# Kernel optimization log

Hardware: AMD Instinct MI355X
Metric: run time of the kernel (lower is better)

The kernel has to match this reference:

```python
import jax, jax.numpy as jnp
import numpy as np
import math

# Static config derived from init_kwargs
B, L, D, H, NL = 256, 256, 128, 2, 2
E = D // H                       # 64
F = L // 2 + 1                   # 129 rfft bins
SR = 0.6                         # sample_ratio (> 1/n_layers)
STEP = (F * (1.0 - SR)) // (NL - 1)          # 51.0, python float floor-div as in torch code
LEFTS = [int(F * (1.0 - SR) - k * STEP) for k in range(NL)]   # [51, 0]
RIGHTS = [int(F - k * STEP) for k in range(NL)]               # [129, 78]
TOPK = max(int(1 * math.log(L)), 1)          # factor=1 -> 5
NUM_TOTAL = 100000                           # user_num + item_num
SPATIAL_RATIO = 0.1
INV_SQRT_E = 1.0 / math.sqrt(E)
INV_SQRT_2 = 1.0 / math.sqrt(2.0)


def setup_inputs() -> dict:
    key = jax.random.key(0)
    ks = jax.random.split(key, 12)
    s = 0.05
    return {
        "paths": jax.random.randint(ks[0], (B, L), 0, NUM_TOTAL),
        "lengths": jax.random.randint(ks[1], (B,), 1, L + 1),
        "degrees": jax.random.randint(ks[2], (B,), 0, 64),
        "training": 1,
        "ego_emb": jax.random.normal(ks[3], (NUM_TOTAL + 1, D), jnp.float32) * s,
        "pos_emb": jax.random.normal(ks[4], (L, D), jnp.float32) * s,
        "Wq": jax.random.normal(ks[5], (NL, D, D), jnp.float32) * s,
        "Wk": jax.random.normal(ks[6], (NL, D, D), jnp.float32) * s,
        "Wv": jax.random.normal(ks[7], (NL, D, D), jnp.float32) * s,
        "Wp": jax.random.normal(ks[8], (NL, D, D), jnp.float32) * s,
        "F1": jax.random.normal(ks[9], (NL, D, 2 * D), jnp.float32) * s,
        "F2": jax.random.normal(ks[10], (NL, 2 * D, D), jnp.float32) * s,
    }


def _hybrid_attention(k, x, mask, Wq, Wk, Wv, Wp):
    # project and split heads: [B,H,E,L]
    def proj(W):
        return (x @ W).reshape(B, L, H, E).transpose(0, 2, 3, 1)
    q, kk, v = proj(Wq), proj(Wk), proj(Wv)
    qf = jnp.fft.rfft(q, axis=-1)   # [B,H,E,F] complex
    kf = jnp.fft.rfft(kk, axis=-1)
    vf = jnp.fft.rfft(v, axis=-1)
    l, r = LEFTS[k], RIGHTS[k]
    # frequency-band attention: band-limited cross-correlation (scatter back == zero-pad)
    res = qf[..., l:r] * jnp.conj(kf[..., l:r])
    box = jnp.zeros(qf.shape, dtype=res.dtype).at[..., l:r].set(res)
    corr = jnp.fft.irfft(box, n=L, axis=-1)          # [B,H,E,L]
    mean_value = jnp.mean(corr, axis=(1, 2))         # [B,L]
    # training branch: global topk delays (shared across batch), roll-based aggregation
    _, delays = jax.lax.top_k(jnp.mean(mean_value, axis=0), TOPK)   # [TOPK]
    weights = mean_value[:, delays]                  # [B,TOPK]
    tmp_corr = jax.nn.softmax(weights, axis=-1)      # [B,TOPK]
    # roll(v, -d) along time == gather at (t + d) % L
    idx = (jnp.arange(L)[None, :] + delays[:, None]) % L            # [TOPK,L]
    gathered = v[:, :, :, idx]                       # [B,H,E,TOPK,L]
    freq = jnp.einsum('bhetl,bt->bhel', gathered, tmp_corr)
    freq = freq.transpose(0, 3, 1, 2).reshape(B, L, D)
    # dual-domain: time attention on band-limited signals (std=True -> same band)
    def band_ifft(f):
        padded = jnp.zeros(f.shape, dtype=f.dtype).at[..., l:r].set(f[..., l:r])
        return jnp.fft.irfft(padded, n=L, axis=-1).transpose(0, 1, 3, 2)   # [B,H,L,E]
    qt, kt, vt = band_ifft(qf), band_ifft(kf), band_ifft(vf)
    scores = jnp.einsum('bhqe,bhke->bhqk', qt, kt) * INV_SQRT_E + mask
    att = jax.nn.softmax(scores, axis=-1)
    spatial = jnp.einsum('bhqk,bhke->bhqe', att, vt).transpose(0, 2, 1, 3).reshape(B, L, D)
    out = (1.0 - SPATIAL_RATIO) * freq + SPATIAL_RATIO * spatial
    return out @ Wp + x


def reference(paths, lengths, degrees, training, ego_emb, pos_emb, Wq, Wk, Wv, Wp, F1, F2):
    del degrees, training  # degrees unused; training branch baked in (training=True)
    x = ego_emb[paths] + pos_emb[None, :, :]         # [B,L,D]
    m = (paths < NUM_TOTAL).astype(jnp.float32)
    mask = ((1.0 - m) * -10000.0)[:, None, None, :]  # [B,1,1,L]
    for k in range(NL):
        a = _hybrid_attention(k, x, mask, Wq[k], Wk[k], Wv[k], Wp[k])
        h = a @ F1[k]
        h = h * 0.5 * (1.0 + jax.lax.erf(h * INV_SQRT_2))   # exact GELU
        x = h @ F2[k]
    # gather last valid position per sequence
    return x[jnp.arange(B), lengths - 1]             # [B,D]
```

## Files before the change

### kernel.cpp

```cpp
#include <hip/hip_runtime.h>
#include <math.h>

#define Bn 256
#define Ln 256
#define Dn 128
#define Hn 2
#define En 64
#define NLn 2
#define TOPKn 5
#define NUM_TOTALn 100000
#define BLD (Bn*Ln*Dn)
#define WT_LAYER 147456

using frag_ab = __attribute__((ext_vector_type(8))) short;
using frag_cd = __attribute__((ext_vector_type(4))) float;

__device__ inline short f2bf(float f) {
    union { float f; unsigned u; } c; c.f = f;
    unsigned r = (c.u + 0x7FFFu + ((c.u >> 16) & 1u)) >> 16;
    return (short)r;
}
__device__ inline float bf2f(short s) {
    union { unsigned u; float f; } c; c.u = ((unsigned)(unsigned short)s) << 16;
    return c.f;
}

__global__ void beacon_kernel(float* out, float v) { out[0] = v; }

__global__ __launch_bounds__(256) void build_G_kernel(short* __restrict__ G) {
    int k = blockIdx.x, t = blockIdx.y, s = threadIdx.x;
    int d = (t - s) & 255;
    int f1 = (k == 0) ? 51 : 1;
    int f2 = (k == 0) ? 127 : 77;
    float acc;
    if (d == 0) {
        acc = 2.0f * (float)(f2 - f1 + 1);
    } else {
        const float c = 3.14159265358979323846f / 256.0f;
        int ahi = (d * (2 * f2 + 1)) & 511;
        int alo = (d * (2 * f1 - 1)) & 511;
        acc = (sinf(c * (float)ahi) - sinf(c * (float)alo)) / sinf(c * (float)d);
    }
    acc += (k == 0) ? ((d & 1) ? -1.0f : 1.0f)
                    : 1.0f;
    G[((size_t)k * 256 + t) * 256 + s] = f2bf(acc * (1.0f / 256.0f));
}

__global__ __launch_bounds__(256) void build_x_kernel(const int* __restrict__ paths,
                                                      const float* __restrict__ ego,
                                                      const float* __restrict__ pos,
                                                      short* __restrict__ x) {
    int base = (blockIdx.x * 256 + threadIdx.x) * 4;
    int d = base & 127;
    int bl = base >> 7;
    int t = bl & 255;
    float4 e = *(const float4*)(ego + (size_t)paths[bl] * Dn + d);
    float4 p = *(const float4*)(pos + t * Dn + d);
    short4 s;
    s.x = f2bf(e.x + p.x); s.y = f2bf(e.y + p.y);
    s.z = f2bf(e.z + p.z); s.w = f2bf(e.w + p.w);
    *(short4*)&x[base] = s;
}

__global__ __launch_bounds__(256) void wtrans_all_kernel(
        const float* __restrict__ Wq, const float* __restrict__ Wk,
        const float* __restrict__ Wv, const float* __restrict__ Wp,
        const float* __restrict__ F1, const float* __restrict__ F2,
        short* __restrict__ Wt) {
    int z = blockIdx.y;
    int idx = blockIdx.x * 256 + threadIdx.x;
    short* WtL = Wt + (size_t)z * WT_LAYER;
    if (idx < 65536) {
        int which = idx >> 14, local = idx & 16383;
        const float* src = (which == 0) ? Wq : (which == 1) ? Wk
                         : (which == 2) ? Wv : Wp;
        float scale = (which == 3) ? 0.1f : 1.0f;
        int n = local & 127, k = local >> 7;
        WtL[(which << 14) + n * 128 + k] = f2bf(scale * src[(size_t)z * 16384 + local]);
    } else if (idx < 98304) {
        int local = idx - 65536;
        int n = local & 255, k = local >> 8;
        WtL[65536 + n * 128 + k] = f2bf(F1[(size_t)z * 32768 + local]);
    } else {
        int local = idx - 98304;
        int n = local & 127, k = local >> 7;
        WtL[98304 + n * 256 + k] = f2bf(F2[(size_t)z * 32768 + local]);
    }
}

template<bool BT_FAST, bool GELU_EPI>
__global__ __launch_bounds__(256)
void mfma_gemm_kernel(const short* A, const short* Bp, short* C, const short* R,
                      int K, int lda, int ldb, int ldc, int ldr,
                      long long sA, long long sB, long long sC, long long sR,
                      long long sCsplit, float alpha, float beta) {
    int bz = blockIdx.z;
    A += (size_t)bz * sA; C += (size_t)bz * sC;
    if (R) R += (size_t)bz * sR;
    const short* Bt = Bp + (size_t)bz * sB;
    const int m0 = blockIdx.x * 128, n0 = blockIdx.y * 128;
    int n0c = n0;
    if (sCsplit) { C += (size_t)blockIdx.y * sCsplit; n0c = 0; }
    __shared__ short As[128 * 40];
    __shared__ short Bs[128 * 40];
    int tid = threadIdx.x;
    int lane = tid & 63, wave = tid >> 6;
    int wr = (wave >> 1) * 64, wc = (wave & 1) * 64;
    int l15 = lane & 15, qd = lane >> 4;

    frag_cd zero4 = {0.f, 0.f, 0.f, 0.f};
    frag_cd acc[4][4];
    #pragma unroll
    for (int i = 0; i < 4; i++)
        #pragma unroll
        for (int j = 0; j < 4; j++) acc[i][j] = zero4;

    int arow = tid >> 1, acg = (tid & 1) * 16;
    int bnrow = tid >> 1, bcg = (tid & 1) * 16;
    int bkk = tid & 31, bnb = (tid >> 5) * 16;

    int4 pa0, pa1, pb0, pb1;
    {
        const short* ap = A + (size_t)(m0 + arow) * lda + acg;
        pa0 = *(const int4*)ap; pa1 = *(const int4*)(ap + 8);
        if (BT_FAST) {
            const short* bp = Bt + (size_t)(n0 + bnrow) * ldb + bcg;
            pb0 = *(const int4*)bp; pb1 = *(const int4*)(bp + 8);
        } else {
            const short* bp = Bt + (size_t)bkk * ldb + n0 + bnb;
            pb0 = *(const int4*)bp; pb1 = *(const int4*)(bp + 8);
        }
    }

    for (int k0 = 0; k0 < K; k0 += 32) {
        __syncthreads();
        *(int4*)&As[arow * 40 + acg] = pa0;
        *(int4*)&As[arow * 40 + acg + 8] = pa1;
        if (BT_FAST) {
            *(int4*)&Bs[bnrow * 40 + bcg] = pb0;
            *(int4*)&Bs[bnrow * 40 + bcg + 8] = pb1;
        } else {
            short tmp[16];
            *(int4*)&tmp[0] = pb0; *(int4*)&tmp[8] = pb1;
            #pragma unroll
            for (int i = 0; i < 16; i++) Bs[(bnb + i) * 40 + bkk] = tmp[i];
        }
        __syncthreads();
        if (k0 + 32 < K) {
            const short* ap = A + (size_t)(m0 + arow) * lda + k0 + 32 + acg;
            pa0 = *(const int4*)ap; pa1 = *(const int4*)(ap + 8);
            if (BT_FAST) {
                const short* bp = Bt + (size_t)(n0 + bnrow) * ldb + k0 + 32 + bcg;
                pb0 = *(const int4*)bp; pb1 = *(const int4*)(bp + 8);
            } else {
                const short* bp = Bt + (size_t)(k0 + 32 + bkk) * ldb + n0 + bnb;
                pb0 = *(const int4*)bp; pb1 = *(const int4*)(bp + 8);
            }
        }
        frag_ab af[4], bf[4];
        #pragma unroll
        for (int ms = 0; ms < 4; ms++)
            af[ms] = *(frag_ab*)&As[(wr + ms * 16 + l15) * 40 + qd * 8];
        #pragma unroll
        for (int ns = 0; ns < 4; ns++)
            bf[ns] = *(frag_ab*)&Bs[(wc + ns * 16 + l15) * 40 + qd * 8];
        #pragma unroll
        for (int ms = 0; ms < 4; ms++)
            #pragma unroll
            for (int ns = 0; ns < 4; ns++)
                acc[ms][ns] = __builtin_amdgcn_mfma_f32_16x16x32_bf16(
                    bf[ns], af[ms], acc[ms][ns], 0, 0, 0);
    }
    #pragma unroll
    for (int ms = 0; ms < 4; ms++) {
        int m = m0 + wr + ms * 16 + l15;
        #pragma unroll
        for (int ns = 0; ns < 4; ns++) {
            int nb = wc + ns * 16 + qd * 4;
            float v[4];
            #pragma unroll
            for (int r = 0; r < 4; r++) v[r] = alpha * acc[ms][ns][r];
            if (R) {
                short4 r4 = *(const short4*)&R[(size_t)m * ldr + n0 + nb];
                v[0] += beta * bf2f(r4.x); v[1] += beta * bf2f(r4.y);
                v[2] += beta * bf2f(r4.z); v[3] += beta * bf2f(r4.w);
            }
            if (GELU_EPI) {
                #pragma unroll
                for (int r = 0; r < 4; r++)
                    v[r] = v[r] * 0.5f * (1.0f + erff(v[r] * 0.70710678118654752f));
            }
            short4 o;
            o.x = f2bf(v[0]); o.y = f2bf(v[1]); o.z = f2bf(v[2]); o.w = f2bf(v[3]);
            *(short4*)&C[(size_t)m * ldc + n0c + nb] = o;
        }
    }
}

static inline void mgemm(hipStream_t s, const short* A, const short* B, short* C,
                         const short* R, int M, int N, int K,
                         int lda, int ldb, int ldc, int ldr,
                         long long sA, long long sB, long long sC, long long sR,
                         int batch, float alpha, float beta, bool btFast, bool gelu,
                         long long sCsplit = 0) {
    dim3 grid(M / 128, N / 128, batch), block(256);
    if (btFast) {
        if (gelu) mfma_gemm_kernel<true, true ><<<grid, block, 0, s>>>(A, B, C, R, K, lda, ldb, ldc, ldr, sA, sB, sC, sR, sCsplit, alpha, beta);
        else      mfma_gemm_kernel<true, false><<<grid, block, 0, s>>>(A, B, C, R, K, lda, ldb, ldc, ldr, sA, sB, sC, sR, sCsplit, alpha, beta);
    } else {
        if (gelu) mfma_gemm_kernel<false, true ><<<grid, block, 0, s>>>(A, B, C, R, K, lda, ldb, ldc, ldr, sA, sB, sC, sR, sCsplit, alpha, beta);
        else      mfma_gemm_kernel<false, false><<<grid, block, 0, s>>>(A, B, C, R, K, lda, ldb, ldc, ldr, sA, sB, sC, sR, sCsplit, alpha, beta);
    }
}

template<bool DUAL, bool GELU_EPI, bool MIXA>
__global__ __launch_bounds__(512)
void bgemm_kernel(const short* __restrict__ A1, const short* __restrict__ B1, int K1,
                  const short* __restrict__ A2, const short* __restrict__ B2, int K2,
                  short* C, const short* __restrict__ R, int ldc, int ldr,
                  long long sCsplit,
                  const float* __restrict__ tc, const int* __restrict__ delays) {
    const int m0 = blockIdx.x * 256;
    int n0c;
    if (sCsplit) { C += (size_t)blockIdx.y * sCsplit; n0c = 0; }
    else         { n0c = blockIdx.y * 128; }
    __shared__ short As[256 * 40];
    __shared__ short Bs[128 * 40];
    int tid = threadIdx.x;
    int lane = tid & 63, wave = tid >> 6;
    int wr = (wave & 3) * 64, wc = (wave >> 2) * 64;
    int l15 = lane & 15, qd = lane >> 4;

    float wj[TOPKn]; int dj[TOPKn];
    if (MIXA) {
        #pragma unroll
        for (int j = 0; j < TOPKn; j++) {
            wj[j] = tc[blockIdx.x * TOPKn + j];
            dj[j] = delays[j];
        }
    }

    frag_cd zero4 = {0.f, 0.f, 0.f, 0.f};
    frag_cd acc[4][4];
    #pragma unroll
    for (int i = 0; i < 4; i++)
        #pragma unroll
        for (int j = 0; j < 4; j++) acc[i][j] = zero4;

    int arow = tid >> 1, acg = (tid & 1) * 16;
    int brow = tid >> 2, bcg = (tid & 3) * 8;

    #pragma unroll
    for (int pass = 0; pass < (DUAL ? 2 : 1); pass++) {
        const short* A = pass ? A2 : A1;
        const short* Bb = (pass ? B2 : B1);
        int K = pass ? K2 : K1;
        const bool domix = MIXA && (pass == 0);
        const short* Bt = Bb + (size_t)blockIdx.y * 128 * K;
        const short* xb = A + ((size_t)m0 << 7);
        int4 pa0, pa1, pb0;
        {
            if (!domix) {
                const short* ap = A + (size_t)(m0 + arow) * K + acg;
                pa0 = *(const int4*)ap; pa1 = *(const int4*)(ap + 8);
            }
            pb0 = *(const int4*)(Bt + (size_t)brow * K + bcg);
        }
        for (int k0 = 0; k0 < K; k0 += 32) {
            __syncthreads();
            if (domix) {
                #pragma unroll
                for (int c = 0; c < 2; c++) {
                    int col = k0 + acg + c * 8;
                    float m8[8] = {0.f, 0.f, 0.f, 0.f, 0.f, 0.f, 0.f, 0.f};
                    #pragma unroll
                    for (int j = 0; j < TOPKn; j++) {
                        frag_ab v = *(const frag_ab*)(xb + (((arow + dj[j]) & 255) << 7) + col);
                        #pragma unroll
                        for (int i = 0; i < 8; i++) m8[i] += wj[j] * bf2f(v[i]);
                    }
                    frag_ab o;
                    #pragma unroll
                    for (int i = 0; i < 8; i++) o[i] = f2bf(m8[i]);
                    *(frag_ab*)&As[arow * 40 + acg + c * 8] = o;
                }
            } else {
                *(int4*)&As[arow * 40 + acg] = pa0;
                *(int4*)&As[arow * 40 + acg + 8] = pa1;
            }
            *(int4*)&Bs[brow * 40 + bcg] = pb0;
            __syncthreads();
            if (k0 + 32 < K) {
                if (!domix) {
                    const short* ap = A + (size_t)(m0 + arow) * K + k0 + 32 + acg;
                    pa0 = *(const int4*)ap; pa1 = *(const int4*)(ap + 8);
                }
                pb0 = *(const int4*)(Bt + (size_t)brow * K + k0 + 32 + bcg);
            }
            frag_ab af[4], bf[4];
            #pragma unroll
            for (int ms = 0; ms < 4; ms++)
                af[ms] = *(frag_ab*)&As[(wr + ms * 16 + l15) * 40 + qd * 8];
            #pragma unroll
            for (int ns = 0; ns < 4; ns++)
                bf[ns] = *(frag_ab*)&Bs[(wc + ns * 16 + l15) * 40 + qd * 8];
            #pragma unroll
            for (int ms = 0; ms < 4; ms++)
                #pragma unroll
                for (int ns = 0; ns < 4; ns++)
                    acc[ms][ns] = __builtin_amdgcn_mfma_f32_16x16x32_bf16(
                        bf[ns], af[ms], acc[ms][ns], 0, 0, 0);
        }
    }
    #pragma unroll
    for (int ms = 0; ms < 4; ms++) {
        int m = m0 + wr + ms * 16 + l15;
        #pragma unroll
        for (int ns = 0; ns < 4; ns++) {
            int nb = wc + ns * 16 + qd * 4;
            float v[4];
            #pragma unroll
            for (int r = 0; r < 4; r++) v[r] = acc[ms][ns][r];
            if (R) {
                short4 r4 = *(const short4*)&R[(size_t)m * ldr + n0c + nb];
                v[0] += bf2f(r4.x); v[1] += bf2f(r4.y);
                v[2] += bf2f(r4.z); v[3] += bf2f(r4.w);
            }
            if (GELU_EPI) {
                #pragma unroll
                for (int r = 0; r < 4; r++)
                    v[r] = v[r] * 0.5f * (1.0f + erff(v[r] * 0.70710678118654752f));
            }
            short4 o;
            o.x = f2bf(v[0]); o.y = f2bf(v[1]); o.z = f2bf(v[2]); o.w = f2bf(v[3]);
            *(short4*)&C[(size_t)m * ldc + n0c + nb] = o;
        }
    }
}

__global__ __launch_bounds__(512, 4) void attn_kernel(short* q,
        const short* __restrict__ kb, const short* __restrict__ vf,
        const int* __restrict__ paths, float* __restrict__ mv2) {
    int h = blockIdx.x, b = blockIdx.y;
    __shared__ short SB[256 * 72];
    __shared__ short ks[64 * 72];
    __shared__ short vT[80 * 72];
    __shared__ float masks[256];
    __shared__ float mvpart[512];
    int tid = threadIdx.x;
    int lane = tid & 63, wave = tid >> 6;
    int l15 = lane & 15, qd = lane >> 4;
    if (tid < 256) masks[tid] = (paths[b * 256 + tid] < NUM_TOTALn) ? 0.0f : -10000.0f;
    {
        int e0 = tid * 2;
        #pragma unroll
        for (int i = 0; i < 2; i++) {
            int e = e0 + i;
            int row = 64 + (e >> 6), col = e & 63;
            vT[row * 72 + col] = (row == 64) ? (short)0x3F80 : (short)0;
        }
    }
    short* qg = q + ((size_t)b << 15) + (size_t)h * 64;
    const short* kg = kb + ((size_t)b << 15) + (size_t)h * 64;
    const short* vg = vf + ((size_t)b << 15) + (size_t)h * 64;

    #pragma unroll
    for (int p = 0; p < 4; p++) {
        int chunk = p * 512 + tid;
        int r = chunk >> 3, cb = (chunk & 7) * 8;
        *(frag_ab*)&SB[r * 72 + cb] = *(const frag_ab*)(qg + (size_t)r * 128 + cb);
    }
    __syncthreads();
    int myrow = wave * 32;
    frag_ab aq[2][2];
    #pragma unroll
    for (int mt = 0; mt < 2; mt++)
        #pragma unroll
        for (int hf = 0; hf < 2; hf++)
            aq[mt][hf] = *(frag_ab*)&SB[(myrow + mt * 16 + l15) * 72 + hf * 32 + qd * 8];

    frag_cd zero4 = {0.f, 0.f, 0.f, 0.f};
    frag_cd oacc[2][5];
    #pragma unroll
    for (int mt = 0; mt < 2; mt++)
        #pragma unroll
        for (int et = 0; et < 5; et++) oacc[mt][et] = zero4;
    float macc = 0.0f;
    int tau = tid & 255, half = tid >> 8;

    for (int jt = 0; jt < 4; jt++) {
        __syncthreads();
        {
            int r = tid >> 3, cb = (tid & 7) * 8;
            *(frag_ab*)&ks[r * 72 + cb] =
                *(const frag_ab*)(kg + (size_t)(jt * 64 + r) * 128 + cb);
            frag_ab v8 = *(const frag_ab*)(vg + (size_t)(jt * 64 + r) * 128 + cb);
            int swz = (((r >> 3) ^ (cb >> 3)) << 3) + (r & 7);
            #pragma unroll
            for (int i = 0; i < 8; i++) vT[(cb + i) * 72 + swz] = v8[i];
        }
        __syncthreads();
        #pragma unroll
        for (int mt = 0; mt < 2; mt++) {
            #pragma unroll
            for (int nt = 0; nt < 4; nt++) {
                frag_ab b0 = *(frag_ab*)&ks[(nt * 16 + l15) * 72 + qd * 8];
                frag_ab b1 = *(frag_ab*)&ks[(nt * 16 + l15) * 72 + 32 + qd * 8];
                frag_cd c = zero4;
                c = __builtin_amdgcn_mfma_f32_16x16x32_bf16(aq[mt][0], b0, c, 0, 0, 0);
                c = __builtin_amdgcn_mfma_f32_16x16x32_bf16(aq[mt][1], b1, c, 0, 0, 0);
                int keyLocal = nt * 16 + l15;
                #pragma unroll
                for (int r = 0; r < 4; r++) {
                    int row = myrow + mt * 16 + qd * 4 + r;
                    int tt = (row - jt * 64 - keyLocal) & 255;
                    SB[tt * 66 + keyLocal] = f2bf(c[r] * 0.125f);
                }
            }
        }
        __syncthreads();
        {
            const int* SD32 = (const int*)&SB[tau * 66 + half * 32];
            #pragma unroll
            for (int i = 0; i < 16; i++) {
                int pk = SD32[i];
                macc += bf2f((short)(pk & 0xFFFF)) + bf2f((short)(pk >> 16));
            }
        }
        #pragma unroll
        for (int mt = 0; mt < 2; mt++) {
            int row = myrow + mt * 16 + l15;
            #pragma unroll
            for (int hf = 0; hf < 2; hf++) {
                int kl0 = hf * 32 + qd * 8;
                frag_ab pfrag;
                #pragma unroll
                for (int j = 0; j < 8; j++) {
                    int kl = kl0 + j;
                    int tt = (row - jt * 64 - kl) & 255;
                    float s = bf2f(SB[tt * 66 + kl]);
                    pfrag[j] = f2bf(__expf(s + masks[jt * 64 + kl]));
                }
                #pragma unroll
                for (int et = 0; et < 5; et++) {
                    int e = et * 16 + l15;
                    int blk = (hf * 4 + qd) ^ ((e >> 3) & 7);
                    frag_ab bv = *(frag_ab*)&vT[e * 72 + (blk << 3)];
                    oacc[mt][et] = __builtin_amdgcn_mfma_f32_16x16x32_bf16(pfrag, bv, oacc[mt][et], 0, 0, 0);
                }
            }
        }
    }
    __syncthreads();
    mvpart[tid] = macc;
    __syncthreads();
    if (tid < 256)
        mv2[(size_t)h * 65536 + b * 256 + tid] =
            (mvpart[tid] + mvpart[tid + 256]) * 0.0625f;
    #pragma unroll
    for (int mt = 0; mt < 2; mt++) {
        #pragma unroll
        for (int r = 0; r < 4; r++) {
            float l = oacc[mt][4][r];
            l = __shfl(l, (lane & 48));
            float inv = 1.0f / l;
            int row = myrow + mt * 16 + qd * 4 + r;
            #pragma unroll
            for (int et = 0; et < 4; et++)
                qg[(size_t)row * 128 + et * 16 + l15] = f2bf(oacc[mt][et][r] * inv);
        }
    }
}

__global__ __launch_bounds__(256) void gm_reduce_kernel(const float* __restrict__ mv2,
                                                        float* __restrict__ gm) {
    int tau = blockIdx.x;
    int b = threadIdx.x;
    __shared__ float red[256];
    red[b] = mv2[b * 256 + tau] + mv2[65536 + b * 256 + tau];
    __syncthreads();
    for (int s = 128; s > 0; s >>= 1) { if (b < s) red[b] += red[b + s]; __syncthreads(); }
    if (b == 0) gm[tau] = red[0] * (1.0f / 256.0f);
}

__global__ __launch_bounds__(256) void topk_softmax_kernel(const float* __restrict__ gm,
                                                           const float* __restrict__ mv2,
                                                           int* __restrict__ delays,
                                                           float* __restrict__ tc) {
    __shared__ float vsh[4];
    __shared__ int ish[4];
    __shared__ int dsh[TOPKn];
    int tid = threadIdx.x;
    int lane = tid & 63, wave = tid >> 6;
    float v = gm[tid];
    for (int t = 0; t < TOPKn; t++) {
        float mv_ = v; int mi = tid;
        #pragma unroll
        for (int s = 32; s > 0; s >>= 1) {
            float v2 = __shfl_xor(mv_, s); int i2 = __shfl_xor(mi, s);
            if (v2 > mv_ || (v2 == mv_ && i2 < mi)) { mv_ = v2; mi = i2; }
        }
        if (lane == 0) { vsh[wave] = mv_; ish[wave] = mi; }
        __syncthreads();
        if (tid == 0) {
            float bv = vsh[0]; int bi = ish[0];
            #pragma unroll
            for (int w = 1; w < 4; w++)
                if (vsh[w] > bv || (vsh[w] == bv && ish[w] < bi)) { bv = vsh[w]; bi = ish[w]; }
            dsh[t] = bi; delays[t] = bi;
        }
        __syncthreads();
        if (tid == dsh[t]) v = -1e30f;
    }
    __syncthreads();
    int b = tid;
    float w[TOPKn];
    float m = -1e30f;
    #pragma unroll
    for (int j = 0; j < TOPKn; j++) {
        w[j] = mv2[b * 256 + dsh[j]] + mv2[65536 + b * 256 + dsh[j]];
        m = fmaxf(m, w[j]);
    }
    float ssum = 0.0f;
    #pragma unroll
    for (int j = 0; j < TOPKn; j++) { w[j] = expf(w[j] - m); ssum += w[j]; }
    #pragma unroll
    for (int j = 0; j < TOPKn; j++) tc[b * TOPKn + j] = w[j] / ssum;
}

__global__ __launch_bounds__(256) void gather_out_kernel(const short* __restrict__ x,
                                                         const int* __restrict__ lengths,
                                                         float* __restrict__ out) {
    int idx = blockIdx.x * 256 + threadIdx.x;
    int d = idx & 127;
    int b = idx >> 7;
    out[idx] = bf2f(x[((size_t)b << 15) + (size_t)(lengths[b] - 1) * Dn + d]);
}

extern "C" void kernel_launch(void* const* d_in, const int* in_sizes, int n_in,
                              void* d_out, int out_size, void* d_ws, size_t ws_size,
                              hipStream_t stream) {
    const int* paths    = (const int*)d_in[0];
    const int* lengths  = (const int*)d_in[1];
    const float* ego    = (const float*)d_in[4];
    const float* pos    = (const float*)d_in[5];
    const float* Wq     = (const float*)d_in[6];
    const float* Wk     = (const float*)d_in[7];
    const float* Wv     = (const float*)d_in[8];
    const float* Wp     = (const float*)d_in[9];
    const float* F1     = (const float*)d_in[10];
    const float* F2     = (const float*)d_in[11];
    float* out = (float*)d_out;

    const size_t need = (size_t)5 * BLD * 2 + 131072 * 2 + 131072 * 4
                        + 256 * 4 + 1280 * 4 + 16 * 4 + (size_t)NLn * WT_LAYER * 2;
    if (ws_size < need) {
        beacon_kernel<<<dim3(1), dim3(1), 0, stream>>>(out, (float)(ws_size >> 20));
        return;
    }

    short* x    = (short*)d_ws;
    short* q    = x + (size_t)1 * BLD;
    short* kb   = x + (size_t)2 * BLD;
    short* vf   = x + (size_t)3 * BLD;
    short* x5   = x + (size_t)4 * BLD;
    short* Gb   = x + (size_t)5 * BLD;
    float* mv   = (float*)(Gb + 131072);
    float* gm   = mv + 131072;
    float* tc   = gm + 256;
    int* delays = (int*)(tc + 1280);
    short* Wt   = (short*)(delays + 16);

    build_G_kernel<<<dim3(2, 256), dim3(256), 0, stream>>>(Gb);
    build_x_kernel<<<dim3(BLD / 1024), dim3(256), 0, stream>>>(paths, ego, pos, x);

    wtrans_all_kernel<<<dim3(512, NLn), dim3(256), 0, stream>>>(Wq, Wk, Wv, Wp, F1, F2, Wt);
    mgemm(stream, Wt + 49152, Wt + 32768, Wt + 131072, nullptr,
          128, 128, 128, 128, 128, 128, 0,
          WT_LAYER, WT_LAYER, WT_LAYER, 0, NLn,
          9.0f, 0.0f, false, false);

    for (int k = 0; k < NLn; k++) {
        const short* WtL = Wt + (size_t)k * WT_LAYER;
        mgemm(stream, Gb + (size_t)k * 65536, x, x5, nullptr,
              256, 128, 256, 256, 128, 128, 0,
              0, 32768, 32768, 0, 256, 1.0f, 0.0f, false, false);
        bgemm_kernel<false, false, false><<<dim3(256, 3), dim3(512), 0, stream>>>(
            x5, WtL + 0, 128, nullptr, nullptr, 0, q, nullptr, 128, 0,
            (long long)BLD, nullptr, nullptr);

        attn_kernel<<<dim3(2, 256), dim3(512), 0, stream>>>(q, kb, vf, paths, mv);

        gm_reduce_kernel<<<dim3(256), dim3(256), 0, stream>>>(mv, gm);
        topk_softmax_kernel<<<dim3(1), dim3(256), 0, stream>>>(gm, mv, delays, tc);

        bgemm_kernel<true, false, true><<<dim3(256, 1), dim3(512), 0, stream>>>(
            x, WtL + 131072, 128, q, WtL + 49152, 128, kb, x, 128, 128, 0,
            tc, delays);
        bgemm_kernel<false, true, false><<<dim3(256, 2), dim3(512), 0, stream>>>(
            kb, WtL + 65536, 128, nullptr, nullptr, 0, vf, nullptr, 256, 0, 0,
            nullptr, nullptr);
        bgemm_kernel<false, false, false><<<dim3(256, 1), dim3(512), 0, stream>>>(
            vf, WtL + 98304, 256, nullptr, nullptr, 0, x, nullptr, 128, 0, 0,
            nullptr, nullptr);
    }

    gather_out_kernel<<<dim3((Bn * Dn) / 256), dim3(256), 0, stream>>>(x, lengths, out);
}
```

Measured before the change: 392.5 us.

## Fuse band-filter GEMM with Q/K/V projection, keeping filtered activations in LDS

Replaces the per-batch filter GEMM (G @ x, written to a global x5 buffer) and the following Q/K/V projection GEMM with one kernel per batch element. The filtered 256x128 tile is kept in shared memory and reused for all three projections. This removes a global write and read of the intermediate plus one launch. In exchange it uses much more LDS per block (about 98 KB), which lowers occupancy, and the grid shrinks to 256 blocks that each run the three projections in sequence.

After: 378.4 us. 3.6% less time.

```diff
diff --git a/kernel.cpp b/kernel.cpp
--- a/kernel.cpp
+++ b/kernel.cpp
@@ -213,6 +213,129 @@
     }
 }
 
+__global__ __launch_bounds__(512)
+void filtproj_kernel(const short* __restrict__ G, const short* __restrict__ x,
+                     const short* __restrict__ W, short* __restrict__ q) {
+    int b = blockIdx.x;
+    __shared__ short As[256 * 40];
+    __shared__ short Bs[128 * 40];
+    __shared__ short xf[256 * 136];
+    int tid = threadIdx.x;
+    int lane = tid & 63, wave = tid >> 6;
+    int wr = (wave & 3) * 64, wc = (wave >> 2) * 64;
+    int l15 = lane & 15, qd = lane >> 4;
+    const short* xb = x + ((size_t)b << 15);
+
+    frag_cd zero4 = {0.f, 0.f, 0.f, 0.f};
+    frag_cd acc[4][4];
+    #pragma unroll
+    for (int i = 0; i < 4; i++)
+        #pragma unroll
+        for (int j = 0; j < 4; j++) acc[i][j] = zero4;
+
+    int arow = tid >> 1, acg = (tid & 1) * 16;
+    int bkk = tid & 31, bnb = (tid >> 5) * 16;
+
+    int4 pa0, pa1, pb0, pb1;
+    {
+        const short* ap = G + (size_t)arow * 256 + acg;
+        pa0 = *(const int4*)ap; pa1 = *(const int4*)(ap + 8);
+        if (tid < 256) {
+            const short* bp = xb + (size_t)bkk * 128 + bnb;
+            pb0 = *(const int4*)bp; pb1 = *(const int4*)(bp + 8);
+        }
+    }
+    for (int k0 = 0; k0 < 256; k0 += 32) {
+        __syncthreads();
+        *(int4*)&As[arow * 40 + acg] = pa0;
+        *(int4*)&As[arow * 40 + acg + 8] = pa1;
+        if (tid < 256) {
+            short tmp[16];
+            *(int4*)&tmp[0] = pb0; *(int4*)&tmp[8] = pb1;
+            #pragma unroll
+            for (int i = 0; i < 16; i++) Bs[(bnb + i) * 40 + bkk] = tmp[i];
+        }
+        __syncthreads();
+        if (k0 + 32 < 256) {
+            const short* ap = G + (size_t)arow * 256 + k0 + 32 + acg;
+            pa0 = *(const int4*)ap; pa1 = *(const int4*)(ap + 8);
+            if (tid < 256) {
+                const short* bp = xb + (size_t)(k0 + 32 + bkk) * 128 + bnb;
+                pb0 = *(const int4*)bp; pb1 = *(const int4*)(bp + 8);
+            }
+        }
+        frag_ab af[4], bf[4];
+        #pragma unroll
+        for (int ms = 0; ms < 4; ms++)
+            af[ms] = *(frag_ab*)&As[(wr + ms * 16 + l15) * 40 + qd * 8];
+        #pragma unroll
+        for (int ns = 0; ns < 4; ns++)
+            bf[ns] = *(frag_ab*)&Bs[(wc + ns * 16 + l15) * 40 + qd * 8];
+        #pragma unroll
+        for (int ms = 0; ms < 4; ms++)
+            #pragma unroll
+            for (int ns = 0; ns < 4; ns++)
+                acc[ms][ns] = __builtin_amdgcn_mfma_f32_16x16x32_bf16(
+                    bf[ns], af[ms], acc[ms][ns], 0, 0, 0);
+    }
+    #pragma unroll
+    for (int ms = 0; ms < 4; ms++) {
+        int m = wr + ms * 16 + l15;
+        #pragma unroll
+        for (int ns = 0; ns < 4; ns++) {
+            int nb = wc + ns * 16 + qd * 4;
+            short4 o;
+            o.x = f2bf(acc[ms][ns][0]); o.y = f2bf(acc[ms][ns][1]);
+            o.z = f2bf(acc[ms][ns][2]); o.w = f2bf(acc[ms][ns][3]);
+            *(short4*)&xf[m * 136 + nb] = o;
+        }
+    }
+
+    int brow = tid >> 2, bcg = (tid & 3) * 8;
+    #pragma unroll 1
+    for (int y = 0; y < 3; y++) {
+        const short* Bt = W + y * 16384;
+        #pragma unroll
+        for (int i = 0; i < 4; i++)
+            #pragma unroll
+            for (int j = 0; j < 4; j++) acc[i][j] = zero4;
+        int4 pb = *(const int4*)(Bt + (size_t)brow * 128 + bcg);
+        for (int k0 = 0; k0 < 128; k0 += 32) {
+            __syncthreads();
+            *(int4*)&Bs[brow * 40 + bcg] = pb;
+            __syncthreads();
+            if (k0 + 32 < 128)
+                pb = *(const int4*)(Bt + (size_t)brow * 128 + k0 + 32 + bcg);
+            frag_ab af[4], bf[4];
+            #pragma unroll
+            for (int ms = 0; ms < 4; ms++)
+                af[ms] = *(frag_ab*)&xf[(wr + ms * 16 + l15) * 136 + k0 + qd * 8];
+            #pragma unroll
+            for (int ns = 0; ns < 4; ns++)
+                bf[ns] = *(frag_ab*)&Bs[(wc + ns * 16 + l15) * 40 + qd * 8];
+            #pragma unroll
+            for (int ms = 0; ms < 4; ms++)
+                #pragma unroll
+                for (int ns = 0; ns < 4; ns++)
+                    acc[ms][ns] = __builtin_amdgcn_mfma_f32_16x16x32_bf16(
+                        bf[ns], af[ms], acc[ms][ns], 0, 0, 0);
+        }
+        short* Cy = q + (size_t)y * BLD + ((size_t)b << 15);
+        #pragma unroll
+        for (int ms = 0; ms < 4; ms++) {
+            int m = wr + ms * 16 + l15;
+            #pragma unroll
+            for (int ns = 0; ns < 4; ns++) {
+                int nb = wc + ns * 16 + qd * 4;
+                short4 o;
+                o.x = f2bf(acc[ms][ns][0]); o.y = f2bf(acc[ms][ns][1]);
+                o.z = f2bf(acc[ms][ns][2]); o.w = f2bf(acc[ms][ns][3]);
+                *(short4*)&Cy[(size_t)m * 128 + nb] = o;
+            }
+        }
+    }
+}
+
 template<bool DUAL, bool GELU_EPI, bool MIXA>
 __global__ __launch_bounds__(512)
 void bgemm_kernel(const short* __restrict__ A1, const short* __restrict__ B1, int K1,
@@ -582,12 +705,8 @@
 
     for (int k = 0; k < NLn; k++) {
         const short* WtL = Wt + (size_t)k * WT_LAYER;
-        mgemm(stream, Gb + (size_t)k * 65536, x, x5, nullptr,
-              256, 128, 256, 256, 128, 128, 0,
-              0, 32768, 32768, 0, 256, 1.0f, 0.0f, false, false);
-        bgemm_kernel<false, false, false><<<dim3(256, 3), dim3(512), 0, stream>>>(
-            x5, WtL + 0, 128, nullptr, nullptr, 0, q, nullptr, 128, 0,
-            (long long)BLD, nullptr, nullptr);
+        filtproj_kernel<<<dim3(256), dim3(512), 0, stream>>>(
+            Gb + (size_t)k * 65536, x, WtL, q);
 
         attn_kernel<<<dim3(2, 256), dim3(512), 0, stream>>>(q, kb, vf, paths, mv);
 
```
